# Kernel tuning notes

Measured on AMD Instinct MI355X. Metric: run time of the kernel, lower is better.

Reference implementation:

```python
import jax, jax.numpy as jnp
import numpy as np

B, S, H, D = 1, 8192, 16, 128
DIM = H * D
POSITION = S - 1  # decode at the last cache slot -> attends over full 8K cache
W_STD = 0.02      # realistic init scale so attention logits are well-conditioned


def setup_inputs() -> dict:
    key = jax.random.key(0)
    ks = jax.random.split(key, 7)
    x = jax.random.normal(ks[0], (B, 1, DIM), dtype=jnp.float32)
    k_cache = jax.random.normal(ks[1], (B, S, H, D), dtype=jnp.float32)
    v_cache = jax.random.normal(ks[2], (B, S, H, D), dtype=jnp.float32)
    w_q = jax.random.normal(ks[3], (DIM, DIM), dtype=jnp.float32) * W_STD
    w_k = jax.random.normal(ks[4], (DIM, DIM), dtype=jnp.float32) * W_STD
    w_v = jax.random.normal(ks[5], (DIM, DIM), dtype=jnp.float32) * W_STD
    w_o = jax.random.normal(ks[6], (DIM, DIM), dtype=jnp.float32) * W_STD
    return {"x": x, "k_cache": k_cache, "v_cache": v_cache,
            "w_q": w_q, "w_k": w_k, "w_v": w_v, "w_o": w_o,
            "position": POSITION}


def reference(x, k_cache, v_cache, w_q, w_k, w_v, w_o, position):
    # decode_step: single token x -> q/k/v projections (torch Linear: y = x @ W.T)
    b = x.shape[0]
    h, d = k_cache.shape[2], k_cache.shape[3]
    dim = x.shape[-1]
    q = (x @ w_q.T).reshape(b, 1, h, d)      # [B,1,H,D]
    k_new = (x @ w_k.T).reshape(b, 1, h, d)
    v_new = (x @ w_v.T).reshape(b, 1, h, d)
    # append current token's K/V into the cache at `position` (static Python int)
    k_cache = k_cache.at[:, position:position + 1].set(k_new)
    v_cache = v_cache.at[:, position:position + 1].set(v_new)
    k_past = k_cache[:, :position + 1]       # [B,K,H,D], K = position+1
    v_past = v_cache[:, :position + 1]
    scale = 1.0 / np.sqrt(d).astype(np.float32)
    # single-query causal decode: the query at `position` may attend to all
    # cached keys [0..position], so no mask is needed.
    scores = jnp.einsum('bqhd,bkhd->bhqk', q, k_past) * scale  # [B,H,1,K]
    attn = jax.nn.softmax(scores, axis=-1)
    out = jnp.einsum('bhqk,bkhd->bqhd', attn, v_past).reshape(b, 1, dim)
    return out @ w_o.T                        # [B,1,dim]
```

## Files before the change

kernel.cpp:

```cpp
#include <hip/hip_runtime.h>
#include <math.h>

namespace {
constexpr int kDim = 2048;
constexpr int kH = 16;
constexpr int kD = 128;
constexpr int kS = 8192;
constexpr int kChunk = 128;
constexpr int kNChunk = kS / kChunk;
constexpr float kScale = 0.08838834764831843f;
}

__global__ __launch_bounds__(256) void qkv_gemv(
    const float* __restrict__ x, const float* __restrict__ wq,
    const float* __restrict__ wk, const float* __restrict__ wv,
    float* __restrict__ qkv)
{
    const int wid  = (blockIdx.x << 2) | ((int)threadIdx.x >> 6);
    const int lane = threadIdx.x & 63;
    const float* W;
    int r = wid;
    if (r < kDim)            { W = wq; }
    else if (r < 2 * kDim)   { W = wk; r -= kDim; }
    else                     { W = wv; r -= 2 * kDim; }
    const float4* wrow = reinterpret_cast<const float4*>(W + (size_t)r * kDim);
    const float4* x4   = reinterpret_cast<const float4*>(x);
    float4 wr[8], xv[8];
#pragma unroll
    for (int k = 0; k < 8; ++k) wr[k] = wrow[(k << 6) + lane];
#pragma unroll
    for (int k = 0; k < 8; ++k) xv[k] = x4[(k << 6) + lane];
    float acc = 0.f;
#pragma unroll
    for (int k = 0; k < 8; ++k)
        acc += wr[k].x * xv[k].x + wr[k].y * xv[k].y
             + wr[k].z * xv[k].z + wr[k].w * xv[k].w;
#pragma unroll
    for (int off = 32; off; off >>= 1) acc += __shfl_xor(acc, off, 64);
    if (lane == 0) qkv[wid] = acc;
}

__global__ __launch_bounds__(256) void attn_fused(
    const float* __restrict__ k_cache, const float* __restrict__ v_cache,
    const float* __restrict__ qkv, const int* __restrict__ pos_p,
    float* __restrict__ part)
{
    const int h     = blockIdx.x >> 6;
    const int chunk = blockIdx.x & (kNChunk - 1);
    const int wave  = threadIdx.x >> 6;
    const int lane  = threadIdx.x & 63;
    const int half  = lane >> 5;
    const int l32   = lane & 31;
    const int pos   = pos_p[0];
    const int s0    = chunk * kChunk;
    const int kb    = s0 + wave * 32;

    __shared__ float  sm[4], sl[4];
    __shared__ float4 sacc[4][32];

    const float4* knew4 = reinterpret_cast<const float4*>(qkv + kDim + h * kD);
    const float4* vnew4 = reinterpret_cast<const float4*>(qkv + 2 * kDim + h * kD);
    const float4* kp0 = reinterpret_cast<const float4*>(k_cache)
                        + (size_t)(kb + half) * (kH * kD / 4) + h * (kD / 4) + l32;
    const float4* vp0 = reinterpret_cast<const float4*>(v_cache)
                        + (size_t)(kb + half) * (kH * kD / 4) + h * (kD / 4) + l32;
    const bool tail = (kb + 32 > pos);

    const float4 q4 = reinterpret_cast<const float4*>(qkv + h * kD)[l32];

    float p[16];
    {
        float4 kv[8];
#pragma unroll
        for (int g = 0; g < 2; ++g) {
            if (!tail) {
#pragma unroll
                for (int j = 0; j < 8; ++j)
                    kv[j] = kp0[(size_t)(g * 8 + j) * 1024];
            } else {
#pragma unroll
                for (int j = 0; j < 8; ++j) {
                    const int key = kb + 2 * (g * 8 + j) + half;
                    kv[j] = (key == pos) ? knew4[l32] : kp0[(size_t)(g * 8 + j) * 1024];
                }
            }
#pragma unroll
            for (int j = 0; j < 8; ++j)
                p[g * 8 + j] = kv[j].x * q4.x + kv[j].y * q4.y
                             + kv[j].z * q4.z + kv[j].w * q4.w;
        }
    }
#pragma unroll
    for (int mask = 1; mask <= 16; mask <<= 1) {
#pragma unroll
        for (int i = 0; i < 16; ++i)
            p[i] += __shfl_xor(p[i], mask, 32);
    }
    if (!tail) {
#pragma unroll
        for (int i = 0; i < 16; ++i) p[i] *= kScale;
    } else {
#pragma unroll
        for (int i = 0; i < 16; ++i) {
            const int key = kb + 2 * i + half;
            p[i] = (key <= pos) ? p[i] * kScale : -INFINITY;
        }
    }

    float mw = p[0];
#pragma unroll
    for (int i = 1; i < 16; ++i) mw = fmaxf(mw, p[i]);
    mw = fmaxf(mw, __shfl_xor(mw, 32, 64));
    float es = 0.f;
    float e[16];
#pragma unroll
    for (int i = 0; i < 16; ++i) {
        e[i] = (p[i] > -INFINITY) ? __expf(p[i] - mw) : 0.f;
        es += e[i];
    }
    const float lw = es + __shfl_xor(es, 32, 64);

    float4 acc = make_float4(0.f, 0.f, 0.f, 0.f);
    {
        float4 vv[8];
#pragma unroll
        for (int g = 0; g < 2; ++g) {
            if (!tail) {
#pragma unroll
                for (int j = 0; j < 8; ++j)
                    vv[j] = vp0[(size_t)(g * 8 + j) * 1024];
            } else {
#pragma unroll
                for (int j = 0; j < 8; ++j) {
                    const int key = kb + 2 * (g * 8 + j) + half;
                    vv[j] = (key == pos) ? vnew4[l32] : vp0[(size_t)(g * 8 + j) * 1024];
                }
            }
#pragma unroll
            for (int j = 0; j < 8; ++j) {
                const float w = e[g * 8 + j];
                acc.x += w * vv[j].x;
                acc.y += w * vv[j].y;
                acc.z += w * vv[j].z;
                acc.w += w * vv[j].w;
            }
        }
    }
    acc.x += __shfl_xor(acc.x, 32, 64);
    acc.y += __shfl_xor(acc.y, 32, 64);
    acc.z += __shfl_xor(acc.z, 32, 64);
    acc.w += __shfl_xor(acc.w, 32, 64);

    if (half == 0) sacc[wave][l32] = acc;
    if (lane == 0) { sm[wave] = mw; sl[wave] = lw; }
    __syncthreads();

    if (wave == 0 && lane < 32) {
        const float M = fmaxf(fmaxf(sm[0], sm[1]), fmaxf(sm[2], sm[3]));
        float L = 0.f;
        float4 A = make_float4(0.f, 0.f, 0.f, 0.f);
#pragma unroll
        for (int w = 0; w < 4; ++w) {
            if (sl[w] > 0.f) {
                const float f = __expf(sm[w] - M);
                const float4 a = sacc[w][l32];
                L   += sl[w] * f;
                A.x += a.x * f; A.y += a.y * f; A.z += a.z * f; A.w += a.w * f;
            }
        }
        float* pp = part + (size_t)(h * kNChunk + chunk) * (kD + 2);
        reinterpret_cast<float4*>(pp)[l32] = A;
        if (l32 == 0) { pp[kD] = M; pp[kD + 1] = L; }
    }
}

__global__ __launch_bounds__(128) void combine_partials(
    const float* __restrict__ part, float* __restrict__ o_out)
{
    const int h = blockIdx.x;
    const int t = threadIdx.x;
    __shared__ float f_lds[kNChunk];
    __shared__ float Lg;

    float mc = -INFINITY, lc = 0.f;
    if (t < kNChunk) {
        const float* pp = part + (size_t)(h * kNChunk + t) * (kD + 2);
        mc = pp[kD];
        lc = pp[kD + 1];
    }
    if (t < 64) {
        float Mg = mc;
#pragma unroll
        for (int m = 32; m; m >>= 1) Mg = fmaxf(Mg, __shfl_xor(Mg, m, 64));
        const float f = (lc > 0.f) ? __expf(mc - Mg) : 0.f;
        f_lds[t] = f;
        float lf = lc * f;
#pragma unroll
        for (int m = 32; m; m >>= 1) lf += __shfl_xor(lf, m, 64);
        if (t == 0) Lg = lf;
    }
    __syncthreads();

    float O = 0.f;
    const float* base = part + (size_t)h * kNChunk * (kD + 2) + t;
#pragma unroll 8
    for (int c = 0; c < kNChunk; ++c)
        O += base[(size_t)c * (kD + 2)] * f_lds[c];
    o_out[h * kD + t] = O / Lg;
}

__global__ __launch_bounds__(256) void out_gemv(
    const float* __restrict__ o, const float* __restrict__ wo,
    float* __restrict__ out)
{
    const int wid  = (blockIdx.x << 2) | ((int)threadIdx.x >> 6);
    const int lane = threadIdx.x & 63;
    const float4* wrow = reinterpret_cast<const float4*>(wo + (size_t)wid * kDim);
    const float4* x4   = reinterpret_cast<const float4*>(o);
    float4 wr[8], xv[8];
#pragma unroll
    for (int k = 0; k < 8; ++k) wr[k] = wrow[(k << 6) + lane];
#pragma unroll
    for (int k = 0; k < 8; ++k) xv[k] = x4[(k << 6) + lane];
    float acc = 0.f;
#pragma unroll
    for (int k = 0; k < 8; ++k)
        acc += wr[k].x * xv[k].x + wr[k].y * xv[k].y
             + wr[k].z * xv[k].z + wr[k].w * xv[k].w;
#pragma unroll
    for (int off = 32; off; off >>= 1) acc += __shfl_xor(acc, off, 64);
    if (lane == 0) out[wid] = acc;
}

extern "C" void kernel_launch(void* const* d_in, const int* in_sizes, int n_in,
                              void* d_out, int out_size, void* d_ws, size_t ws_size,
                              hipStream_t stream)
{
    const float* x       = (const float*)d_in[0];
    const float* k_cache = (const float*)d_in[1];
    const float* v_cache = (const float*)d_in[2];
    const float* wq      = (const float*)d_in[3];
    const float* wk      = (const float*)d_in[4];
    const float* wv      = (const float*)d_in[5];
    const float* wo      = (const float*)d_in[6];
    const int*   pos     = (const int*)d_in[7];
    float* out = (float*)d_out;

    float* ws    = (float*)d_ws;
    float* qkv   = ws;
    float* part  = qkv + 3 * kDim;
    float* o_out = part + kH * kNChunk * (kD + 2);

    qkv_gemv<<<3 * kDim / 4, 256, 0, stream>>>(x, wq, wk, wv, qkv);
    attn_fused<<<kH * kNChunk, 256, 0, stream>>>(k_cache, v_cache, qkv, pos, part);
    combine_partials<<<kH, 128, 0, stream>>>(part, o_out);
    out_gemv<<<kDim / 4, 256, 0, stream>>>(o_out, wo, out);
}
```

Measured before the change: 50.14 us.

## Halve attention chunk size to double block count and prefetch V earlier

Result: slower. 51.94 us (+3.6%).

```diff
diff --git a/kernel.cpp b/kernel.cpp
--- a/kernel.cpp
+++ b/kernel.cpp
@@ -6,7 +6,7 @@
 constexpr int kH = 16;
 constexpr int kD = 128;
 constexpr int kS = 8192;
-constexpr int kChunk = 128;
+constexpr int kChunk = 64;
 constexpr int kNChunk = kS / kChunk;
 constexpr float kScale = 0.08838834764831843f;
 }
@@ -45,7 +45,7 @@
     const float* __restrict__ qkv, const int* __restrict__ pos_p,
     float* __restrict__ part)
 {
-    const int h     = blockIdx.x >> 6;
+    const int h     = blockIdx.x >> 7;
     const int chunk = blockIdx.x & (kNChunk - 1);
     const int wave  = threadIdx.x >> 6;
     const int lane  = threadIdx.x & 63;
@@ -53,7 +53,7 @@
     const int l32   = lane & 31;
     const int pos   = pos_p[0];
     const int s0    = chunk * kChunk;
-    const int kb    = s0 + wave * 32;
+    const int kb    = s0 + wave * 16;
 
     __shared__ float  sm[4], sl[4];
     __shared__ float4 sacc[4][32];
@@ -64,44 +64,52 @@
                         + (size_t)(kb + half) * (kH * kD / 4) + h * (kD / 4) + l32;
     const float4* vp0 = reinterpret_cast<const float4*>(v_cache)
                         + (size_t)(kb + half) * (kH * kD / 4) + h * (kD / 4) + l32;
-    const bool tail = (kb + 32 > pos);
+    const bool tail = (kb + 16 > pos);
 
     const float4 q4 = reinterpret_cast<const float4*>(qkv + h * kD)[l32];
 
-    float p[16];
+    float p[8];
     {
         float4 kv[8];
-#pragma unroll
-        for (int g = 0; g < 2; ++g) {
-            if (!tail) {
-#pragma unroll
-                for (int j = 0; j < 8; ++j)
-                    kv[j] = kp0[(size_t)(g * 8 + j) * 1024];
-            } else {
-#pragma unroll
-                for (int j = 0; j < 8; ++j) {
-                    const int key = kb + 2 * (g * 8 + j) + half;
-                    kv[j] = (key == pos) ? knew4[l32] : kp0[(size_t)(g * 8 + j) * 1024];
-                }
+        if (!tail) {
+#pragma unroll
+            for (int j = 0; j < 8; ++j) kv[j] = kp0[(size_t)j * 1024];
+        } else {
+#pragma unroll
+            for (int j = 0; j < 8; ++j) {
+                const int key = kb + 2 * j + half;
+                kv[j] = (key == pos) ? knew4[l32] : kp0[(size_t)j * 1024];
             }
-#pragma unroll
-            for (int j = 0; j < 8; ++j)
-                p[g * 8 + j] = kv[j].x * q4.x + kv[j].y * q4.y
-                             + kv[j].z * q4.z + kv[j].w * q4.w;
-        }
-    }
+        }
+#pragma unroll
+        for (int j = 0; j < 8; ++j)
+            p[j] = kv[j].x * q4.x + kv[j].y * q4.y + kv[j].z * q4.z + kv[j].w * q4.w;
+    }
+
+    float4 vv[8];
+    if (!tail) {
+#pragma unroll
+        for (int j = 0; j < 8; ++j) vv[j] = vp0[(size_t)j * 1024];
+    } else {
+#pragma unroll
+        for (int j = 0; j < 8; ++j) {
+            const int key = kb + 2 * j + half;
+            vv[j] = (key == pos) ? vnew4[l32] : vp0[(size_t)j * 1024];
+        }
+    }
+
 #pragma unroll
     for (int mask = 1; mask <= 16; mask <<= 1) {
 #pragma unroll
-        for (int i = 0; i < 16; ++i)
+        for (int i = 0; i < 8; ++i)
             p[i] += __shfl_xor(p[i], mask, 32);
     }
     if (!tail) {
 #pragma unroll
-        for (int i = 0; i < 16; ++i) p[i] *= kScale;
+        for (int i = 0; i < 8; ++i) p[i] *= kScale;
     } else {
 #pragma unroll
-        for (int i = 0; i < 16; ++i) {
+        for (int i = 0; i < 8; ++i) {
             const int key = kb + 2 * i + half;
             p[i] = (key <= pos) ? p[i] * kScale : -INFINITY;
         }
@@ -109,42 +117,24 @@
 
     float mw = p[0];
 #pragma unroll
-    for (int i = 1; i < 16; ++i) mw = fmaxf(mw, p[i]);
+    for (int i = 1; i < 8; ++i) mw = fmaxf(mw, p[i]);
     mw = fmaxf(mw, __shfl_xor(mw, 32, 64));
+    float e[8];
     float es = 0.f;
-    float e[16];
-#pragma unroll
-    for (int i = 0; i < 16; ++i) {
+#pragma unroll
+    for (int i = 0; i < 8; ++i) {
         e[i] = (p[i] > -INFINITY) ? __expf(p[i] - mw) : 0.f;
         es += e[i];
     }
     const float lw = es + __shfl_xor(es, 32, 64);
 
     float4 acc = make_float4(0.f, 0.f, 0.f, 0.f);
-    {
-        float4 vv[8];
-#pragma unroll
-        for (int g = 0; g < 2; ++g) {
-            if (!tail) {
-#pragma unroll
-                for (int j = 0; j < 8; ++j)
-                    vv[j] = vp0[(size_t)(g * 8 + j) * 1024];
-            } else {
-#pragma unroll
-                for (int j = 0; j < 8; ++j) {
-                    const int key = kb + 2 * (g * 8 + j) + half;
-                    vv[j] = (key == pos) ? vnew4[l32] : vp0[(size_t)(g * 8 + j) * 1024];
-                }
-            }
-#pragma unroll
-            for (int j = 0; j < 8; ++j) {
-                const float w = e[g * 8 + j];
-                acc.x += w * vv[j].x;
-                acc.y += w * vv[j].y;
-                acc.z += w * vv[j].z;
-                acc.w += w * vv[j].w;
-            }
-        }
+#pragma unroll
+    for (int j = 0; j < 8; ++j) {
+        acc.x += e[j] * vv[j].x;
+        acc.y += e[j] * vv[j].y;
+        acc.z += e[j] * vv[j].z;
+        acc.w += e[j] * vv[j].w;
     }
     acc.x += __shfl_xor(acc.x, 32, 64);
     acc.y += __shfl_xor(acc.y, 32, 64);
@@ -177,29 +167,31 @@
 __global__ __launch_bounds__(128) void combine_partials(
     const float* __restrict__ part, float* __restrict__ o_out)
 {
-    const int h = blockIdx.x;
-    const int t = threadIdx.x;
-    __shared__ float f_lds[kNChunk];
-    __shared__ float Lg;
-
-    float mc = -INFINITY, lc = 0.f;
-    if (t < kNChunk) {
-        const float* pp = part + (size_t)(h * kNChunk + t) * (kD + 2);
-        mc = pp[kD];
-        lc = pp[kD + 1];
-    }
-    if (t < 64) {
-        float Mg = mc;
-#pragma unroll
-        for (int m = 32; m; m >>= 1) Mg = fmaxf(Mg, __shfl_xor(Mg, m, 64));
-        const float f = (lc > 0.f) ? __expf(mc - Mg) : 0.f;
-        f_lds[t] = f;
-        float lf = lc * f;
-#pragma unroll
-        for (int m = 32; m; m >>= 1) lf += __shfl_xor(lf, m, 64);
-        if (t == 0) Lg = lf;
-    }
+    const int h    = blockIdx.x;
+    const int t    = threadIdx.x;
+    const int wave = t >> 6;
+    const int lane = t & 63;
+    __shared__ float wred[2], wsum[2], f_lds[kNChunk];
+
+    const float* pp = part + (size_t)(h * kNChunk + t) * (kD + 2);
+    const float mc = pp[kD];
+    const float lc = pp[kD + 1];
+
+    float mg = mc;
+#pragma unroll
+    for (int m = 32; m; m >>= 1) mg = fmaxf(mg, __shfl_xor(mg, m, 64));
+    if (lane == 0) wred[wave] = mg;
     __syncthreads();
+    const float Mg = fmaxf(wred[0], wred[1]);
+
+    const float f = (lc > 0.f) ? __expf(mc - Mg) : 0.f;
+    f_lds[t] = f;
+    float lf = lc * f;
+#pragma unroll
+    for (int m = 32; m; m >>= 1) lf += __shfl_xor(lf, m, 64);
+    if (lane == 0) wsum[wave] = lf;
+    __syncthreads();
+    const float Lg = wsum[0] + wsum[1];
 
     float O = 0.f;
     const float* base = part + (size_t)h * kNChunk * (kD + 2) + t;
```
